# Performance work log

Measured on AMD Instinct MI355X. Metric: run time of the kernel, lower is better.

The kernel has to match this reference:

```python
import jax, jax.numpy as jnp
import numpy as np

NA, NQ, FDIM, NC, HID = 512, 4096, 2, 16, 64
CUTOFF = 6.0
GAMMA = 10.0
BOX = 12.0


def setup_inputs() -> dict:
    key = jax.random.key(0)
    ks = jax.random.split(key, 16)
    s = lambda k, shp, fan: jax.random.normal(k, shp, jnp.float32) * (1.0 / np.sqrt(fan))
    return {
        "atom_pos": jax.random.uniform(ks[0], (NA, 3), jnp.float32) * BOX,
        "atom_feat": jax.random.normal(ks[1], (NA, FDIM), jnp.float32),
        "query_pos": jax.random.uniform(ks[2], (NQ, 3), jnp.float32) * BOX,
        "W1": s(ks[3], (FDIM + NC, HID), FDIM + NC), "b1": jnp.zeros((HID,), jnp.float32),
        "W2": s(ks[4], (HID, HID), HID), "b2": jnp.zeros((HID,), jnp.float32),
        "W3": s(ks[5], (HID, HID // 2), HID), "b3": jnp.zeros((HID // 2,), jnp.float32),
        "W4": s(ks[6], (HID // 2, 1), HID // 2), "b4": jnp.zeros((1,), jnp.float32),
        "W5": s(ks[7], (3, 64), 3), "b5": jnp.zeros((64,), jnp.float32),
        "W6": s(ks[8], (64, 3), 64), "b6": jnp.zeros((3,), jnp.float32),
    }


def _forward(atom_pos, atom_feat, query_pos, W1, b1, W2, b2, W3, b3, W4, b4, W5, b5, W6, b6):
    centers = jnp.linspace(0.0, CUTOFF, NC, dtype=jnp.float32)  # RBF centers
    rel = query_pos[:, None, :] - atom_pos[None, :, :]          # (Nq,Na,3)
    dist = jnp.linalg.norm(rel + 1e-12, axis=-1)                 # (Nq,Na) (matches torch.norm(rel+eps))
    mask = (dist <= CUTOFF).astype(dist.dtype)
    rbf = jnp.exp(-GAMMA * (dist[..., None] - centers) ** 2)     # (Nq,Na,Nc)
    feat_b = jnp.broadcast_to(atom_feat[None], (query_pos.shape[0],) + atom_feat.shape)
    atom_input = jnp.concatenate([feat_b, rbf], axis=-1)         # (Nq,Na,F+Nc)
    h = jax.nn.relu(atom_input @ W1 + b1)
    h = jax.nn.relu(h @ W2 + b2)                                 # (Nq,Na,H)
    scalar_w = (jax.nn.relu(h @ W3 + b3) @ W4 + b4)[..., 0] * mask  # (Nq,Na)
    dir_vec = rel / (dist[..., None] + 1e-12)                    # (Nq,Na,3)
    weighted = jnp.einsum('qa,qad->qd', scalar_w, dir_vec)       # (Nq,3)
    out = jax.nn.relu(weighted @ W5 + b5) @ W6 + b6              # (Nq,3)
    return out


def reference(atom_pos, atom_feat, query_pos, W1, b1, W2, b2, W3, b3, W4, b4, W5, b5, W6, b6):
    return _forward(atom_pos, atom_feat, query_pos, W1, b1, W2, b2, W3, b3, W4, b4, W5, b5, W6, b6)
```

## Files before the change

### kernel.cpp

```cpp
#include <hip/hip_runtime.h>
#include <math.h>


typedef _Float16 f16x8 __attribute__((ext_vector_type(8)));
typedef _Float16 f16x4 __attribute__((ext_vector_type(4)));
typedef _Float16 f16x2 __attribute__((ext_vector_type(2)));
typedef float    f32x4 __attribute__((ext_vector_type(4)));

#define CAP 352
#define XP2 72
#define NT  2

__global__ __launch_bounds__(64) void repack_kernel(
    const float* __restrict__ W1, const float* __restrict__ b1,
    const float* __restrict__ W2, const float* __restrict__ b2,
    const float* __restrict__ W3, const float* __restrict__ b3,
    const float* __restrict__ W4, char* __restrict__ ws)
{
    const int b = blockIdx.x, l = threadIdx.x;
    const int col = l & 15, quad = l >> 4;
    if (b < 16) {
        f16x8 v;
        #pragma unroll
        for (int j = 0; j < 8; ++j) {
            const int k = quad*8 + j;
            float x;
            if (b < 4) {
                const int mt = b;
                x = (k < 18) ? W1[k*64 + mt*16 + col]
                             : (k == 18 ? b1[mt*16 + col] : 0.0f);
            } else if (b < 12) {
                const int kc = (b-4) >> 2, mt = (b-4) & 3;
                x = W2[(kc*32 + k)*64 + mt*16 + col];
            } else {
                const int kc = (b-12) >> 1, mt = (b-12) & 1;
                x = W3[(kc*32 + k)*32 + mt*16 + col];
            }
            v[j] = (_Float16)x;
        }
        *(f16x8*)(ws + (b*64 + l)*16) = v;
    } else {
        const int d = b - 16;
        float o[4];
        #pragma unroll
        for (int rr = 0; rr < 4; ++rr) {
            const int idx = quad*4 + rr;
            if (d < 4)      o[rr] = b2[d*16 + idx];
            else if (d < 6) o[rr] = b3[(d-4)*16 + idx];
            else            o[rr] = W4[(d-6)*16 + idx];
        }
        *(float4*)(ws + 16384 + (d*64 + l)*16) = make_float4(o[0],o[1],o[2],o[3]);
    }
}

__global__ __launch_bounds__(256, 1) void aqfn_kernel(
    const float* __restrict__ atom_pos,
    const float* __restrict__ atom_feat,
    const float* __restrict__ query_pos,
    const float* __restrict__ b4,
    const float* __restrict__ W5, const float* __restrict__ b5,
    const float* __restrict__ W6, const float* __restrict__ b6,
    const char*  __restrict__ ws,
    float* __restrict__ out)
{
    __shared__ __align__(16) float4   rbuf[CAP];
    __shared__ __align__(16) f16x2    fbuf[CAP];
    __shared__ __align__(16) _Float16 exch[4][NT][16*XP2];
    __shared__ float wred[4][3];
    __shared__ int   wcnt[4];

    const int tid  = threadIdx.x;
    const int wave = __builtin_amdgcn_readfirstlane(tid >> 6);
    const int lane = tid & 63;
    const int col  = lane & 15;
    const int quad = lane >> 4;
    const int q    = blockIdx.x;

    const f16x8*  wsf = (const f16x8*)ws;
    const float4* wsb = (const float4*)(ws + 16384);
    f16x8 w1f[4], w2f[2][4], w3f[2][2];
    #pragma unroll
    for (int mt = 0; mt < 4; ++mt) w1f[mt] = wsf[mt*64 + lane];
    #pragma unroll
    for (int kc = 0; kc < 2; ++kc)
        #pragma unroll
        for (int mt = 0; mt < 4; ++mt) w2f[kc][mt] = wsf[(4 + kc*4 + mt)*64 + lane];
    #pragma unroll
    for (int kc = 0; kc < 2; ++kc)
        #pragma unroll
        for (int mt = 0; mt < 2; ++mt) w3f[kc][mt] = wsf[(12 + kc*2 + mt)*64 + lane];
    float4 b2v[4], b3v[2], w4v[2];
    #pragma unroll
    for (int mt = 0; mt < 4; ++mt) b2v[mt] = wsb[mt*64 + lane];
    #pragma unroll
    for (int mt = 0; mt < 2; ++mt) { b3v[mt] = wsb[(4+mt)*64 + lane];
                                     w4v[mt] = wsb[(6+mt)*64 + lane]; }
    const float b4v = b4[0];

    const float qx = query_pos[q*3+0];
    const float qy = query_pos[q*3+1];
    const float qz = query_pos[q*3+2];

    float rxv[2], ryv[2], rzv[2], dv[2], f0v[2], f1v[2];
    unsigned long long msk[2];
    int mycnt = 0;
    #pragma unroll
    for (int it = 0; it < 2; ++it) {
        const int a = wave*128 + it*64 + lane;
        const float rx = qx - atom_pos[a*3+0];
        const float ry = qy - atom_pos[a*3+1];
        const float rz = qz - atom_pos[a*3+2];
        const float ex = __fadd_rn(rx, 1e-12f);
        const float ey = __fadd_rn(ry, 1e-12f);
        const float ez = __fadd_rn(rz, 1e-12f);
        const float dd = __fadd_rn(__fadd_rn(__fmul_rn(ex,ex), __fmul_rn(ey,ey)),
                                   __fmul_rn(ez,ez));
        const float dist = sqrtf(dd);
        rxv[it] = rx; ryv[it] = ry; rzv[it] = rz; dv[it] = dist;
        f0v[it] = atom_feat[a*2+0]; f1v[it] = atom_feat[a*2+1];
        msk[it] = __ballot(dist <= 6.0f);
        mycnt  += (int)__popcll(msk[it]);
    }
    if (lane == 0) wcnt[wave] = mycnt;
    __syncthreads();

    int base = 0, count = 0;
    #pragma unroll
    for (int w = 0; w < 4; ++w) {
        const int c = wcnt[w];
        if (w < wave) base += c;
        count += c;
    }
    if (count > CAP) count = CAP;

    {
        int off0 = base;
        #pragma unroll
        for (int it = 0; it < 2; ++it) {
            const bool in = (msk[it] >> lane) & 1ull;
            const int  p  = off0 + (int)__popcll(msk[it] & ((1ull << lane) - 1ull));
            if (in && p < CAP) {
                rbuf[p] = make_float4(rxv[it], ryv[it], rzv[it], dv[it]);
                fbuf[p] = f16x2{(_Float16)f0v[it], (_Float16)f1v[it]};
            }
            off0 += (int)__popcll(msk[it]);
        }
    }
    __syncthreads();

    float wacc0 = 0.f, wacc1 = 0.f, wacc2 = 0.f;
    const int nchunks = (count + (NT*16 - 1)) / (NT*16);

    #pragma unroll 1
    for (int chunk = wave; chunk < nchunks; chunk += 4) {
        const int row0 = chunk * (NT*16);

        float4 rv[NT]; f16x2 ffv[NT];
        #pragma unroll
        for (int u = 0; u < NT; ++u) {
            int pr = row0 + u*16 + col;
            if (pr >= count) pr = count - 1;
            rv[u]  = rbuf[pr];
            ffv[u] = fbuf[pr];
        }

        f16x8 xa[NT];
        #pragma unroll
        for (int u = 0; u < NT; ++u) {
            const float dist = rv[u].w;
            #pragma unroll
            for (int j = 0; j < 8; ++j) {
                const int k = quad*8 + j;
                const float tt = dist - 0.4f * (float)(k - 2);
                float v = __expf(-10.0f * tt * tt);
                v = (k < 18) ? v : 0.0f;
                _Float16 xv = (_Float16)v;
                if (k == 18) xv = (_Float16)1.0f;
                if (j == 0) xv = (quad == 0) ? ffv[u][0] : xv;
                if (j == 1) xv = (quad == 0) ? ffv[u][1] : xv;
                xa[u][j] = xv;
            }
        }

        #pragma unroll
        for (int u = 0; u < NT; ++u)
            #pragma unroll
            for (int mt = 0; mt < 4; ++mt) {
                f32x4 c = {0.f, 0.f, 0.f, 0.f};
                c = __builtin_amdgcn_mfma_f32_16x16x32_f16(w1f[mt], xa[u], c, 0, 0, 0);
                f16x4 pk = {(_Float16)fmaxf(c[0],0.f), (_Float16)fmaxf(c[1],0.f),
                            (_Float16)fmaxf(c[2],0.f), (_Float16)fmaxf(c[3],0.f)};
                *(f16x4*)&exch[wave][u][col*XP2 + mt*16 + quad*4] = pk;
            }
        f16x8 a2[NT][2];
        #pragma unroll
        for (int u = 0; u < NT; ++u)
            #pragma unroll
            for (int kc = 0; kc < 2; ++kc)
                a2[u][kc] = *(const f16x8*)&exch[wave][u][col*XP2 + kc*32 + quad*8];

        #pragma unroll
        for (int u = 0; u < NT; ++u)
            #pragma unroll
            for (int mt = 0; mt < 4; ++mt) {
                f32x4 c = {b2v[mt].x, b2v[mt].y, b2v[mt].z, b2v[mt].w};
                c = __builtin_amdgcn_mfma_f32_16x16x32_f16(w2f[0][mt], a2[u][0], c, 0, 0, 0);
                c = __builtin_amdgcn_mfma_f32_16x16x32_f16(w2f[1][mt], a2[u][1], c, 0, 0, 0);
                f16x4 pk = {(_Float16)fmaxf(c[0],0.f), (_Float16)fmaxf(c[1],0.f),
                            (_Float16)fmaxf(c[2],0.f), (_Float16)fmaxf(c[3],0.f)};
                *(f16x4*)&exch[wave][u][col*XP2 + mt*16 + quad*4] = pk;
            }
        f16x8 a3[NT][2];
        #pragma unroll
        for (int u = 0; u < NT; ++u)
            #pragma unroll
            for (int kc = 0; kc < 2; ++kc)
                a3[u][kc] = *(const f16x8*)&exch[wave][u][col*XP2 + kc*32 + quad*8];

        #pragma unroll
        for (int u = 0; u < NT; ++u) {
            float s = 0.f;
            #pragma unroll
            for (int mt = 0; mt < 2; ++mt) {
                f32x4 c = {b3v[mt].x, b3v[mt].y, b3v[mt].z, b3v[mt].w};
                c = __builtin_amdgcn_mfma_f32_16x16x32_f16(w3f[0][mt], a3[u][0], c, 0, 0, 0);
                c = __builtin_amdgcn_mfma_f32_16x16x32_f16(w3f[1][mt], a3[u][1], c, 0, 0, 0);
                const float* wv = &w4v[mt].x;
                #pragma unroll
                for (int rr = 0; rr < 4; ++rr)
                    s = fmaf(fmaxf(c[rr], 0.f), wv[rr], s);
            }
            s += __shfl_xor(s, 16);
            s += __shfl_xor(s, 32);
            s += b4v;
            const int  p2  = row0 + u*16 + col;
            const bool vld = (p2 < count);
            const float inv = __builtin_amdgcn_rcpf(rv[u].w + 1e-12f);
            const float wm  = vld ? (s * inv) : 0.f;
            wacc0 = fmaf(wm, rv[u].x, wacc0);
            wacc1 = fmaf(wm, rv[u].y, wacc1);
            wacc2 = fmaf(wm, rv[u].z, wacc2);
        }
    }

    #pragma unroll
    for (int off = 1; off < 64; off <<= 1) {
        wacc0 += __shfl_xor(wacc0, off);
        wacc1 += __shfl_xor(wacc1, off);
        wacc2 += __shfl_xor(wacc2, off);
    }
    if (lane == 0) {
        wred[wave][0] = wacc0 * 0.25f;
        wred[wave][1] = wacc1 * 0.25f;
        wred[wave][2] = wacc2 * 0.25f;
    }
    __syncthreads();

    if (wave == 0) {
        const float v0 = wred[0][0] + wred[1][0] + wred[2][0] + wred[3][0];
        const float v1 = wred[0][1] + wred[1][1] + wred[2][1] + wred[3][1];
        const float v2 = wred[0][2] + wred[1][2] + wred[2][2] + wred[3][2];
        float th = fmaf(v0, W5[lane],
                   fmaf(v1, W5[64+lane],
                   fmaf(v2, W5[128+lane], b5[lane])));
        th = fmaxf(th, 0.f);
        float o0 = th * W6[lane*3+0];
        float o1 = th * W6[lane*3+1];
        float o2 = th * W6[lane*3+2];
        #pragma unroll
        for (int off = 1; off < 64; off <<= 1) {
            o0 += __shfl_xor(o0, off);
            o1 += __shfl_xor(o1, off);
            o2 += __shfl_xor(o2, off);
        }
        if (lane == 0) {
            out[q*3+0] = o0 + b6[0];
            out[q*3+1] = o1 + b6[1];
            out[q*3+2] = o2 + b6[2];
        }
    }
}

extern "C" void kernel_launch(void* const* d_in, const int* in_sizes, int n_in,
                              void* d_out, int out_size, void* d_ws, size_t ws_size,
                              hipStream_t stream) {
    const float* atom_pos  = (const float*)d_in[0];
    const float* atom_feat = (const float*)d_in[1];
    const float* query_pos = (const float*)d_in[2];
    const float* W1 = (const float*)d_in[3];  const float* b1 = (const float*)d_in[4];
    const float* W2 = (const float*)d_in[5];  const float* b2 = (const float*)d_in[6];
    const float* W3 = (const float*)d_in[7];  const float* b3 = (const float*)d_in[8];
    const float* W4 = (const float*)d_in[9];  const float* b4 = (const float*)d_in[10];
    const float* W5 = (const float*)d_in[11]; const float* b5 = (const float*)d_in[12];
    const float* W6 = (const float*)d_in[13]; const float* b6 = (const float*)d_in[14];
    float* out = (float*)d_out;
    char*  ws  = (char*)d_ws;

    hipLaunchKernelGGL(repack_kernel, dim3(24), dim3(64), 0, stream,
                       W1, b1, W2, b2, W3, b3, W4, ws);
    hipLaunchKernelGGL(aqfn_kernel, dim3(4096), dim3(256), 0, stream,
                       atom_pos, atom_feat, query_pos, b4, W5, b5, W6, b6,
                       (const char*)ws, out);
}
```

Before: 118.7 us.

## Process two queries per 512-thread block with shared chunk pool

Each block now handles two queries with eight waves. The in-cutoff atom chunks of both queries go into one combined work list that all eight waves share, which should balance load across waves and halve the per-block weight-loading and launch overhead. In exchange the kernel uses more LDS per block, carries extra per-chunk branching, and adds a larger final reduction across eight waves.

```diff
diff --git a/kernel.cpp b/kernel.cpp
--- a/kernel.cpp
+++ b/kernel.cpp
@@ -53,7 +53,7 @@
     }
 }
 
-__global__ __launch_bounds__(256, 1) void aqfn_kernel(
+__global__ __launch_bounds__(512, 1) void aqfn_kernel(
     const float* __restrict__ atom_pos,
     const float* __restrict__ atom_feat,
     const float* __restrict__ query_pos,
@@ -63,18 +63,19 @@
     const char*  __restrict__ ws,
     float* __restrict__ out)
 {
-    __shared__ __align__(16) float4   rbuf[CAP];
-    __shared__ __align__(16) f16x2    fbuf[CAP];
-    __shared__ __align__(16) _Float16 exch[4][NT][16*XP2];
-    __shared__ float wred[4][3];
-    __shared__ int   wcnt[4];
+    __shared__ __align__(16) float4   rbuf[2][CAP];
+    __shared__ __align__(16) f16x2    fbuf[2][CAP];
+    __shared__ __align__(16) _Float16 exch[8][NT][16*XP2];
+    __shared__ float wred[8][2][3];
+    __shared__ int   wcnt[8];
 
     const int tid  = threadIdx.x;
     const int wave = __builtin_amdgcn_readfirstlane(tid >> 6);
     const int lane = tid & 63;
     const int col  = lane & 15;
     const int quad = lane >> 4;
-    const int q    = blockIdx.x;
+    const int qsel = wave >> 2;
+    const int seg  = wave & 3;
 
     const f16x8*  wsf = (const f16x8*)ws;
     const float4* wsb = (const float4*)(ws + 16384);
@@ -97,16 +98,17 @@
                                      w4v[mt] = wsb[(6+mt)*64 + lane]; }
     const float b4v = b4[0];
 
-    const float qx = query_pos[q*3+0];
-    const float qy = query_pos[q*3+1];
-    const float qz = query_pos[q*3+2];
+    const int qg = blockIdx.x*2 + qsel;
+    const float qx = query_pos[qg*3+0];
+    const float qy = query_pos[qg*3+1];
+    const float qz = query_pos[qg*3+2];
 
     float rxv[2], ryv[2], rzv[2], dv[2], f0v[2], f1v[2];
     unsigned long long msk[2];
     int mycnt = 0;
     #pragma unroll
     for (int it = 0; it < 2; ++it) {
-        const int a = wave*128 + it*64 + lane;
+        const int a = seg*128 + it*64 + lane;
         const float rx = qx - atom_pos[a*3+0];
         const float ry = qy - atom_pos[a*3+1];
         const float rz = qz - atom_pos[a*3+2];
@@ -124,14 +126,15 @@
     if (lane == 0) wcnt[wave] = mycnt;
     __syncthreads();
 
-    int base = 0, count = 0;
+    int base = 0, cnt0 = 0, cnt1 = 0;
     #pragma unroll
     for (int w = 0; w < 4; ++w) {
-        const int c = wcnt[w];
-        if (w < wave) base += c;
-        count += c;
-    }
-    if (count > CAP) count = CAP;
+        cnt0 += wcnt[w];
+        cnt1 += wcnt[4+w];
+        if ((qsel*4 + w) < wave) base += wcnt[qsel*4 + w];
+    }
+    if (cnt0 > CAP) cnt0 = CAP;
+    if (cnt1 > CAP) cnt1 = CAP;
 
     {
         int off0 = base;
@@ -140,28 +143,35 @@
             const bool in = (msk[it] >> lane) & 1ull;
             const int  p  = off0 + (int)__popcll(msk[it] & ((1ull << lane) - 1ull));
             if (in && p < CAP) {
-                rbuf[p] = make_float4(rxv[it], ryv[it], rzv[it], dv[it]);
-                fbuf[p] = f16x2{(_Float16)f0v[it], (_Float16)f1v[it]};
+                rbuf[qsel][p] = make_float4(rxv[it], ryv[it], rzv[it], dv[it]);
+                fbuf[qsel][p] = f16x2{(_Float16)f0v[it], (_Float16)f1v[it]};
             }
             off0 += (int)__popcll(msk[it]);
         }
     }
     __syncthreads();
 
-    float wacc0 = 0.f, wacc1 = 0.f, wacc2 = 0.f;
-    const int nchunks = (count + (NT*16 - 1)) / (NT*16);
+    float acc[2][3] = {{0.f,0.f,0.f},{0.f,0.f,0.f}};
+    const int nch0 = (cnt0 + (NT*16 - 1)) / (NT*16);
+    const int nch1 = (cnt1 + (NT*16 - 1)) / (NT*16);
+    const int ntot = nch0 + nch1;
 
     #pragma unroll 1
-    for (int chunk = wave; chunk < nchunks; chunk += 4) {
-        const int row0 = chunk * (NT*16);
+    for (int g = wave; g < ntot; g += 8) {
+        const int cq    = (g < nch0) ? 0 : 1;
+        const int lc    = (g < nch0) ? g : (g - nch0);
+        const int count = (cq == 0) ? cnt0 : cnt1;
+        const float4* __restrict__ rb = &rbuf[cq][0];
+        const f16x2*  __restrict__ fb = &fbuf[cq][0];
+        const int row0 = lc * (NT*16);
 
         float4 rv[NT]; f16x2 ffv[NT];
         #pragma unroll
         for (int u = 0; u < NT; ++u) {
             int pr = row0 + u*16 + col;
             if (pr >= count) pr = count - 1;
-            rv[u]  = rbuf[pr];
-            ffv[u] = fbuf[pr];
+            rv[u]  = rb[pr];
+            ffv[u] = fb[pr];
         }
 
         f16x8 xa[NT];
@@ -237,29 +247,36 @@
             const bool vld = (p2 < count);
             const float inv = __builtin_amdgcn_rcpf(rv[u].w + 1e-12f);
             const float wm  = vld ? (s * inv) : 0.f;
-            wacc0 = fmaf(wm, rv[u].x, wacc0);
-            wacc1 = fmaf(wm, rv[u].y, wacc1);
-            wacc2 = fmaf(wm, rv[u].z, wacc2);
-        }
-    }
-
-    #pragma unroll
-    for (int off = 1; off < 64; off <<= 1) {
-        wacc0 += __shfl_xor(wacc0, off);
-        wacc1 += __shfl_xor(wacc1, off);
-        wacc2 += __shfl_xor(wacc2, off);
-    }
-    if (lane == 0) {
-        wred[wave][0] = wacc0 * 0.25f;
-        wred[wave][1] = wacc1 * 0.25f;
-        wred[wave][2] = wacc2 * 0.25f;
-    }
+            if (cq == 0) {
+                acc[0][0] = fmaf(wm, rv[u].x, acc[0][0]);
+                acc[0][1] = fmaf(wm, rv[u].y, acc[0][1]);
+                acc[0][2] = fmaf(wm, rv[u].z, acc[0][2]);
+            } else {
+                acc[1][0] = fmaf(wm, rv[u].x, acc[1][0]);
+                acc[1][1] = fmaf(wm, rv[u].y, acc[1][1]);
+                acc[1][2] = fmaf(wm, rv[u].z, acc[1][2]);
+            }
+        }
+    }
+
+    #pragma unroll
+    for (int cq = 0; cq < 2; ++cq)
+        #pragma unroll
+        for (int d = 0; d < 3; ++d) {
+            float v = acc[cq][d];
+            #pragma unroll
+            for (int off = 1; off < 64; off <<= 1) v += __shfl_xor(v, off);
+            if (lane == 0) wred[wave][cq][d] = v * 0.25f;
+        }
     __syncthreads();
 
-    if (wave == 0) {
-        const float v0 = wred[0][0] + wred[1][0] + wred[2][0] + wred[3][0];
-        const float v1 = wred[0][1] + wred[1][1] + wred[2][1] + wred[3][1];
-        const float v2 = wred[0][2] + wred[1][2] + wred[2][2] + wred[3][2];
+    if (wave < 2) {
+        const int cq = wave;
+        float v0 = 0.f, v1 = 0.f, v2 = 0.f;
+        #pragma unroll
+        for (int w = 0; w < 8; ++w) {
+            v0 += wred[w][cq][0]; v1 += wred[w][cq][1]; v2 += wred[w][cq][2];
+        }
         float th = fmaf(v0, W5[lane],
                    fmaf(v1, W5[64+lane],
                    fmaf(v2, W5[128+lane], b5[lane])));
@@ -274,9 +291,10 @@
             o2 += __shfl_xor(o2, off);
         }
         if (lane == 0) {
-            out[q*3+0] = o0 + b6[0];
-            out[q*3+1] = o1 + b6[1];
-            out[q*3+2] = o2 + b6[2];
+            const int qo = blockIdx.x*2 + cq;
+            out[qo*3+0] = o0 + b6[0];
+            out[qo*3+1] = o1 + b6[1];
+            out[qo*3+2] = o2 + b6[2];
         }
     }
 }
@@ -298,7 +316,7 @@
 
     hipLaunchKernelGGL(repack_kernel, dim3(24), dim3(64), 0, stream,
                        W1, b1, W2, b2, W3, b3, W4, ws);
-    hipLaunchKernelGGL(aqfn_kernel, dim3(4096), dim3(256), 0, stream,
+    hipLaunchKernelGGL(aqfn_kernel, dim3(2048), dim3(512), 0, stream,
                        atom_pos, atom_feat, query_pos, b4, W5, b5, W6, b6,
                        (const char*)ws, out);
 }
```

Measured after the change: 141.0 us. 1.19x slower.

## Chain MLP layers in registers via 16x16x16 MFMA, removing LDS exchange

Applied to the files above, without the earlier changes.

Switches from the 16x16x32 MFMA to the 16x16x16 f16 MFMA, whose output layout (4 consecutive rows per lane quad) matches the B-operand layout of the next MFMA. Each layer's ReLU'd output can then feed the next layer straight from registers, with no round trip through the per-wave shared-memory exchange buffer. Weights are repacked into f16x4 fragments with twice as many K-chunks. The cost is twice as many MFMA instructions, each with half the K depth, in exchange for removing the LDS stores and loads between layers.

```diff
diff --git a/kernel.cpp b/kernel.cpp
--- a/kernel.cpp
+++ b/kernel.cpp
@@ -2,13 +2,11 @@
 #include <math.h>
 
 
-typedef _Float16 f16x8 __attribute__((ext_vector_type(8)));
 typedef _Float16 f16x4 __attribute__((ext_vector_type(4)));
 typedef _Float16 f16x2 __attribute__((ext_vector_type(2)));
 typedef float    f32x4 __attribute__((ext_vector_type(4)));
 
 #define CAP 352
-#define XP2 72
 #define NT  2
 
 __global__ __launch_bounds__(64) void repack_kernel(
@@ -19,28 +17,30 @@
 {
     const int b = blockIdx.x, l = threadIdx.x;
     const int col = l & 15, quad = l >> 4;
-    if (b < 16) {
-        f16x8 v;
-        #pragma unroll
-        for (int j = 0; j < 8; ++j) {
-            const int k = quad*8 + j;
+    if (b < 32) {
+        f16x4 v;
+        #pragma unroll
+        for (int j = 0; j < 4; ++j) {
             float x;
-            if (b < 4) {
-                const int mt = b;
+            if (b < 8) {
+                const int kc = b >> 2, mt = b & 3;
+                const int k = kc*16 + quad*4 + j;
                 x = (k < 18) ? W1[k*64 + mt*16 + col]
                              : (k == 18 ? b1[mt*16 + col] : 0.0f);
-            } else if (b < 12) {
-                const int kc = (b-4) >> 2, mt = (b-4) & 3;
-                x = W2[(kc*32 + k)*64 + mt*16 + col];
+            } else if (b < 24) {
+                const int idx = b - 8, kc = idx >> 2, mt = idx & 3;
+                const int k = kc*16 + quad*4 + j;
+                x = W2[k*64 + mt*16 + col];
             } else {
-                const int kc = (b-12) >> 1, mt = (b-12) & 1;
-                x = W3[(kc*32 + k)*32 + mt*16 + col];
+                const int idx = b - 24, kc = idx >> 1, mt = idx & 1;
+                const int k = kc*16 + quad*4 + j;
+                x = W3[k*32 + mt*16 + col];
             }
             v[j] = (_Float16)x;
         }
-        *(f16x8*)(ws + (b*64 + l)*16) = v;
+        *(f16x4*)(ws + (b*64 + l)*8) = v;
     } else {
-        const int d = b - 16;
+        const int d = b - 32;
         float o[4];
         #pragma unroll
         for (int rr = 0; rr < 4; ++rr) {
@@ -51,6 +51,11 @@
         }
         *(float4*)(ws + 16384 + (d*64 + l)*16) = make_float4(o[0],o[1],o[2],o[3]);
     }
+}
+
+__device__ __forceinline__ f16x4 relu_cvt(f32x4 c) {
+    return f16x4{(_Float16)fmaxf(c[0],0.f), (_Float16)fmaxf(c[1],0.f),
+                 (_Float16)fmaxf(c[2],0.f), (_Float16)fmaxf(c[3],0.f)};
 }
 
 __global__ __launch_bounds__(256, 1) void aqfn_kernel(
@@ -63,9 +68,8 @@
     const char*  __restrict__ ws,
     float* __restrict__ out)
 {
-    __shared__ __align__(16) float4   rbuf[CAP];
-    __shared__ __align__(16) f16x2    fbuf[CAP];
-    __shared__ __align__(16) _Float16 exch[4][NT][16*XP2];
+    __shared__ __align__(16) float4 rbuf[CAP];
+    __shared__ __align__(16) f16x2  fbuf[CAP];
     __shared__ float wred[4][3];
     __shared__ int   wcnt[4];
 
@@ -76,19 +80,21 @@
     const int quad = lane >> 4;
     const int q    = blockIdx.x;
 
-    const f16x8*  wsf = (const f16x8*)ws;
+    const f16x4*  wsf = (const f16x4*)ws;
     const float4* wsb = (const float4*)(ws + 16384);
-    f16x8 w1f[4], w2f[2][4], w3f[2][2];
-    #pragma unroll
-    for (int mt = 0; mt < 4; ++mt) w1f[mt] = wsf[mt*64 + lane];
+    f16x4 w1f[2][4], w2f[4][4], w3f[4][2];
     #pragma unroll
     for (int kc = 0; kc < 2; ++kc)
         #pragma unroll
-        for (int mt = 0; mt < 4; ++mt) w2f[kc][mt] = wsf[(4 + kc*4 + mt)*64 + lane];
-    #pragma unroll
-    for (int kc = 0; kc < 2; ++kc)
-        #pragma unroll
-        for (int mt = 0; mt < 2; ++mt) w3f[kc][mt] = wsf[(12 + kc*2 + mt)*64 + lane];
+        for (int mt = 0; mt < 4; ++mt) w1f[kc][mt] = wsf[(kc*4 + mt)*64 + lane];
+    #pragma unroll
+    for (int kc = 0; kc < 4; ++kc)
+        #pragma unroll
+        for (int mt = 0; mt < 4; ++mt) w2f[kc][mt] = wsf[(8 + kc*4 + mt)*64 + lane];
+    #pragma unroll
+    for (int kc = 0; kc < 4; ++kc)
+        #pragma unroll
+        for (int mt = 0; mt < 2; ++mt) w3f[kc][mt] = wsf[(24 + kc*2 + mt)*64 + lane];
     float4 b2v[4], b3v[2], w4v[2];
     #pragma unroll
     for (int mt = 0; mt < 4; ++mt) b2v[mt] = wsb[mt*64 + lane];
@@ -164,58 +170,48 @@
             ffv[u] = fbuf[pr];
         }
 
-        f16x8 xa[NT];
+        f16x4 xa[NT][2];
         #pragma unroll
         for (int u = 0; u < NT; ++u) {
             const float dist = rv[u].w;
             #pragma unroll
-            for (int j = 0; j < 8; ++j) {
-                const int k = quad*8 + j;
-                const float tt = dist - 0.4f * (float)(k - 2);
-                float v = __expf(-10.0f * tt * tt);
-                v = (k < 18) ? v : 0.0f;
-                _Float16 xv = (_Float16)v;
-                if (k == 18) xv = (_Float16)1.0f;
-                if (j == 0) xv = (quad == 0) ? ffv[u][0] : xv;
-                if (j == 1) xv = (quad == 0) ? ffv[u][1] : xv;
-                xa[u][j] = xv;
-            }
-        }
-
+            for (int kc = 0; kc < 2; ++kc)
+                #pragma unroll
+                for (int j = 0; j < 4; ++j) {
+                    const int k = kc*16 + quad*4 + j;
+                    const float tt = dist - 0.4f * (float)(k - 2);
+                    float v = __expf(-10.0f * tt * tt);
+                    v = (k < 18) ? v : 0.0f;
+                    _Float16 xv = (_Float16)v;
+                    if (k == 18) xv = (_Float16)1.0f;
+                    if (k == 0)  xv = ffv[u][0];
+                    if (k == 1)  xv = ffv[u][1];
+                    xa[u][kc][j] = xv;
+                }
+        }
+
+        f16x4 a2[NT][4];
         #pragma unroll
         for (int u = 0; u < NT; ++u)
             #pragma unroll
             for (int mt = 0; mt < 4; ++mt) {
                 f32x4 c = {0.f, 0.f, 0.f, 0.f};
-                c = __builtin_amdgcn_mfma_f32_16x16x32_f16(w1f[mt], xa[u], c, 0, 0, 0);
-                f16x4 pk = {(_Float16)fmaxf(c[0],0.f), (_Float16)fmaxf(c[1],0.f),
-                            (_Float16)fmaxf(c[2],0.f), (_Float16)fmaxf(c[3],0.f)};
-                *(f16x4*)&exch[wave][u][col*XP2 + mt*16 + quad*4] = pk;
-            }
-        f16x8 a2[NT][2];
-        #pragma unroll
-        for (int u = 0; u < NT; ++u)
-            #pragma unroll
-            for (int kc = 0; kc < 2; ++kc)
-                a2[u][kc] = *(const f16x8*)&exch[wave][u][col*XP2 + kc*32 + quad*8];
-
+                c = __builtin_amdgcn_mfma_f32_16x16x16f16(w1f[0][mt], xa[u][0], c, 0, 0, 0);
+                c = __builtin_amdgcn_mfma_f32_16x16x16f16(w1f[1][mt], xa[u][1], c, 0, 0, 0);
+                a2[u][mt] = relu_cvt(c);
+            }
+
+        f16x4 a3[NT][4];
         #pragma unroll
         for (int u = 0; u < NT; ++u)
             #pragma unroll
             for (int mt = 0; mt < 4; ++mt) {
                 f32x4 c = {b2v[mt].x, b2v[mt].y, b2v[mt].z, b2v[mt].w};
-                c = __builtin_amdgcn_mfma_f32_16x16x32_f16(w2f[0][mt], a2[u][0], c, 0, 0, 0);
-                c = __builtin_amdgcn_mfma_f32_16x16x32_f16(w2f[1][mt], a2[u][1], c, 0, 0, 0);
-                f16x4 pk = {(_Float16)fmaxf(c[0],0.f), (_Float16)fmaxf(c[1],0.f),
-                            (_Float16)fmaxf(c[2],0.f), (_Float16)fmaxf(c[3],0.f)};
-                *(f16x4*)&exch[wave][u][col*XP2 + mt*16 + quad*4] = pk;
-            }
-        f16x8 a3[NT][2];
-        #pragma unroll
-        for (int u = 0; u < NT; ++u)
-            #pragma unroll
-            for (int kc = 0; kc < 2; ++kc)
-                a3[u][kc] = *(const f16x8*)&exch[wave][u][col*XP2 + kc*32 + quad*8];
+                #pragma unroll
+                for (int kc = 0; kc < 4; ++kc)
+                    c = __builtin_amdgcn_mfma_f32_16x16x16f16(w2f[kc][mt], a2[u][kc], c, 0, 0, 0);
+                a3[u][mt] = relu_cvt(c);
+            }
 
         #pragma unroll
         for (int u = 0; u < NT; ++u) {
@@ -223,8 +219,9 @@
             #pragma unroll
             for (int mt = 0; mt < 2; ++mt) {
                 f32x4 c = {b3v[mt].x, b3v[mt].y, b3v[mt].z, b3v[mt].w};
-                c = __builtin_amdgcn_mfma_f32_16x16x32_f16(w3f[0][mt], a3[u][0], c, 0, 0, 0);
-                c = __builtin_amdgcn_mfma_f32_16x16x32_f16(w3f[1][mt], a3[u][1], c, 0, 0, 0);
+                #pragma unroll
+                for (int kc = 0; kc < 4; ++kc)
+                    c = __builtin_amdgcn_mfma_f32_16x16x16f16(w3f[kc][mt], a3[u][kc], c, 0, 0, 0);
                 const float* wv = &w4v[mt].x;
                 #pragma unroll
                 for (int rr = 0; rr < 4; ++rr)
@@ -296,7 +293,7 @@
     float* out = (float*)d_out;
     char*  ws  = (char*)d_ws;
 
-    hipLaunchKernelGGL(repack_kernel, dim3(24), dim3(64), 0, stream,
+    hipLaunchKernelGGL(repack_kernel, dim3(40), dim3(64), 0, stream,
                        W1, b1, W2, b2, W3, b3, W4, ws);
     hipLaunchKernelGGL(aqfn_kernel, dim3(4096), dim3(256), 0, stream,
                        atom_pos, atom_feat, query_pos, b4, W5, b5, W6, b6,
```

Measured after the change: 117.3 us. Within noise of the previous version (-1.2%).
